# Kernel optimization log

Measured on AMD Instinct MI355X. Metric: run time of the kernel, lower is better.

Reference implementation:

```python
import jax, jax.numpy as jnp
import numpy as np

B, S, H = 2, 2048, 1024
NH, HD = 16, 64  # num heads, head dim
EPS = 1e-12


def setup_inputs() -> dict:
    key = jax.random.key(0)
    ks = jax.random.split(key, 10)
    sc = 1.0 / np.sqrt(H)
    return {
        "hidden_states": jax.random.normal(ks[0], (B, S, H), jnp.float32),
        "Wq": jax.random.normal(ks[1], (H, H), jnp.float32) * sc,
        "bq": jnp.zeros((H,), jnp.float32),
        "Wk": jax.random.normal(ks[2], (H, H), jnp.float32) * sc,
        "bk": jnp.zeros((H,), jnp.float32),
        "Wv": jax.random.normal(ks[3], (H, H), jnp.float32) * sc,
        "bv": jnp.zeros((H,), jnp.float32),
        "Wo": jax.random.normal(ks[4], (H, H), jnp.float32) * sc,
        "bo": jnp.zeros((H,), jnp.float32),
        "ln_g": jnp.ones((H,), jnp.float32),
        "ln_b": jnp.zeros((H,), jnp.float32),
    }


def reference(hidden_states, Wq, bq, Wk, bk, Wv, bv, Wo, bo, ln_g, ln_b):
    x = hidden_states  # [B,S,H]
    def split_heads(t):
        return t.reshape(B, S, NH, HD).transpose(0, 2, 1, 3)  # [B,NH,S,HD]
    q = split_heads(x @ Wq.T + bq)
    k = split_heads(x @ Wk.T + bk)
    v = split_heads(x @ Wv.T + bv)
    scores = jnp.einsum("bhqd,bhkd->bhqk", q, k) / np.sqrt(HD)
    causal = jnp.tril(jnp.ones((S, S), bool))  # [S,S]
    scores = jnp.where(causal[None, None], scores, -jnp.inf)
    probs = jax.nn.softmax(scores, axis=-1)
    ctx = jnp.einsum("bhqk,bhkd->bhqd", probs, v)
    ctx = ctx.transpose(0, 2, 1, 3).reshape(B, S, H)
    attn_out = ctx @ Wo.T + bo
    y = attn_out + x
    mu = jnp.mean(y, axis=-1, keepdims=True)
    var = jnp.mean((y - mu) ** 2, axis=-1, keepdims=True)
    return (y - mu) / jnp.sqrt(var + EPS) * ln_g + ln_b
```

## Files before the change

### kernel.cpp

```cpp
#include <hip/hip_runtime.h>

#define B_  2
#define S_  2048
#define H_  1024
#define NH_ 16
#define HD_ 64
#define M_  (B_*S_)

typedef __attribute__((ext_vector_type(8))) __bf16 bf16x8;
typedef __attribute__((ext_vector_type(4))) float  f32x4;
typedef __attribute__((ext_vector_type(8))) unsigned short us8;
typedef __attribute__((ext_vector_type(4))) float  fl4;

__device__ __forceinline__ unsigned short f2bf(float f) {
    unsigned int u = __float_as_uint(f);
    u += 0x7fffu + ((u >> 16) & 1u);
    return (unsigned short)(u >> 16);
}

__global__ __launch_bounds__(256) void cast_kernel(
    const float* __restrict__ x,
    const float* __restrict__ wq, const float* __restrict__ wk,
    const float* __restrict__ wv, const float* __restrict__ wo,
    unsigned short* __restrict__ xb, unsigned short* __restrict__ wb) {
    size_t t  = (size_t)blockIdx.x * 256 + threadIdx.x;
    size_t e0 = t * 4;
    const size_t XN = (size_t)M_ * H_;
    const float* src;
    unsigned short* dst;
    if (e0 < XN) { src = x + e0; dst = xb + e0; }
    else {
        size_t j = e0 - XN;
        int w = (int)(j >> 20);
        size_t off = j & ((1u << 20) - 1);
        const float* wp = (w == 0) ? wq : (w == 1) ? wk : (w == 2) ? wv : wo;
        src = wp + off; dst = wb + j;
    }
    fl4 v = *(const fl4*)src;
    ushort4 o;
    o.x = f2bf(v.x); o.y = f2bf(v.y); o.z = f2bf(v.z); o.w = f2bf(v.w);
    *(ushort4*)dst = o;
}

__global__ __launch_bounds__(512) void gemm_qkv(
    const unsigned short* __restrict__ xb, const unsigned short* __restrict__ wb,
    const float* __restrict__ bq, const float* __restrict__ bk,
    const float* __restrict__ bv,
    unsigned short* __restrict__ qb, unsigned short* __restrict__ kbuf,
    unsigned short* __restrict__ vT) {
    __shared__ __align__(16) unsigned short As[128 * 72];
    __shared__ __align__(16) unsigned short Bs[128 * 72];
    const int z = blockIdx.z;
    const unsigned short* W = wb + ((size_t)z << 20);
    const int m0 = blockIdx.x * 128, n0 = blockIdx.y * 128;
    const int t = threadIdx.x, lane = t & 63, w = t >> 6;
    const int wm = w >> 2, wn = w & 3;
    const int quad = lane >> 4, l16 = lane & 15;
    const int sr = t >> 2, sc = (t & 3) * 16;
    const unsigned short* ga = xb + (size_t)(m0 + sr) * H_ + sc;
    const unsigned short* gb = W  + (size_t)(n0 + sr) * H_ + sc;

    us8 a0 = *(const us8*)(ga),     a1 = *(const us8*)(ga + 8);
    us8 b0 = *(const us8*)(gb),     b1 = *(const us8*)(gb + 8);

    f32x4 acc[4][2] = {};
    for (int k0 = 0; k0 < H_; k0 += 64) {
        if (k0) __syncthreads();
        *(us8*)&As[sr * 72 + sc]     = a0;  *(us8*)&As[sr * 72 + sc + 8] = a1;
        *(us8*)&Bs[sr * 72 + sc]     = b0;  *(us8*)&Bs[sr * 72 + sc + 8] = b1;
        __syncthreads();
        if (k0 + 64 < H_) {
            ga += 64; gb += 64;
            a0 = *(const us8*)(ga);  a1 = *(const us8*)(ga + 8);
            b0 = *(const us8*)(gb);  b1 = *(const us8*)(gb + 8);
        }
#pragma unroll
        for (int kk = 0; kk < 64; kk += 32) {
            bf16x8 af[4], bfr[2];
#pragma unroll
            for (int i = 0; i < 4; i++)
                af[i]  = *(const bf16x8*)&As[(wm * 64 + i * 16 + l16) * 72 + kk + quad * 8];
#pragma unroll
            for (int jn = 0; jn < 2; jn++)
                bfr[jn] = *(const bf16x8*)&Bs[(wn * 32 + jn * 16 + l16) * 72 + kk + quad * 8];
#pragma unroll
            for (int mi = 0; mi < 4; mi++)
#pragma unroll
                for (int ni = 0; ni < 2; ni++)
                    acc[mi][ni] = __builtin_amdgcn_mfma_f32_16x16x32_bf16(
                        af[mi], bfr[ni], acc[mi][ni], 0, 0, 0);
        }
    }
    const float* bias = (z == 0) ? bq : (z == 1) ? bk : bv;
    if (z == 2) {
#pragma unroll
        for (int mi = 0; mi < 4; mi++) {
#pragma unroll
            for (int ni = 0; ni < 2; ni++) {
                int col  = n0 + wn * 32 + ni * 16 + l16;
                float bval = bias[col];
                int row0 = m0 + wm * 64 + mi * 16 + quad * 4;
                int bb = row0 >> 11, s0 = row0 & 2047;
                ushort4 pk;
                pk.x = f2bf(acc[mi][ni][0] + bval);
                pk.y = f2bf(acc[mi][ni][1] + bval);
                pk.z = f2bf(acc[mi][ni][2] + bval);
                pk.w = f2bf(acc[mi][ni][3] + bval);
                *(ushort4*)&vT[((size_t)bb * NH_ * HD_ + col) * S_ + s0] = pk;
            }
        }
    } else {
        unsigned short* out = (z == 0) ? qb : kbuf;
        const float qs = (z == 0) ? 0.18033688f : 1.0f;
#pragma unroll
        for (int mi = 0; mi < 4; mi++) {
#pragma unroll
            for (int ni = 0; ni < 2; ni++) {
                int col = n0 + wn * 32 + ni * 16 + l16;
                float bval = bias[col];
#pragma unroll
                for (int r = 0; r < 4; r++) {
                    int row = m0 + wm * 64 + mi * 16 + quad * 4 + r;
                    out[(size_t)row * H_ + col] = f2bf((acc[mi][ni][r] + bval) * qs);
                }
            }
        }
    }
}

__global__ __launch_bounds__(512) void gemm_out(
    const unsigned short* __restrict__ ctxb, const unsigned short* __restrict__ wob,
    const float* __restrict__ bo, const float* __restrict__ x,
    float* __restrict__ y) {
    __shared__ __align__(16) unsigned short As[128 * 72];
    __shared__ __align__(16) unsigned short Bs[128 * 72];
    const int m0 = blockIdx.x * 128, n0 = blockIdx.y * 128;
    const int t = threadIdx.x, lane = t & 63, w = t >> 6;
    const int wm = w >> 2, wn = w & 3;
    const int quad = lane >> 4, l16 = lane & 15;
    const int sr = t >> 2, sc = (t & 3) * 16;
    const unsigned short* ga = ctxb + (size_t)(m0 + sr) * H_ + sc;
    const unsigned short* gb = wob  + (size_t)(n0 + sr) * H_ + sc;

    us8 a0 = *(const us8*)(ga),     a1 = *(const us8*)(ga + 8);
    us8 b0 = *(const us8*)(gb),     b1 = *(const us8*)(gb + 8);

    f32x4 acc[4][2] = {};
    for (int k0 = 0; k0 < H_; k0 += 64) {
        if (k0) __syncthreads();
        *(us8*)&As[sr * 72 + sc]     = a0;  *(us8*)&As[sr * 72 + sc + 8] = a1;
        *(us8*)&Bs[sr * 72 + sc]     = b0;  *(us8*)&Bs[sr * 72 + sc + 8] = b1;
        __syncthreads();
        if (k0 + 64 < H_) {
            ga += 64; gb += 64;
            a0 = *(const us8*)(ga);  a1 = *(const us8*)(ga + 8);
            b0 = *(const us8*)(gb);  b1 = *(const us8*)(gb + 8);
        }
#pragma unroll
        for (int kk = 0; kk < 64; kk += 32) {
            bf16x8 af[4], bfr[2];
#pragma unroll
            for (int i = 0; i < 4; i++)
                af[i]  = *(const bf16x8*)&As[(wm * 64 + i * 16 + l16) * 72 + kk + quad * 8];
#pragma unroll
            for (int jn = 0; jn < 2; jn++)
                bfr[jn] = *(const bf16x8*)&Bs[(wn * 32 + jn * 16 + l16) * 72 + kk + quad * 8];
#pragma unroll
            for (int mi = 0; mi < 4; mi++)
#pragma unroll
                for (int ni = 0; ni < 2; ni++)
                    acc[mi][ni] = __builtin_amdgcn_mfma_f32_16x16x32_bf16(
                        af[mi], bfr[ni], acc[mi][ni], 0, 0, 0);
        }
    }
#pragma unroll
    for (int mi = 0; mi < 4; mi++) {
#pragma unroll
        for (int ni = 0; ni < 2; ni++) {
            int col = n0 + wn * 32 + ni * 16 + l16;
            float bval = bo[col];
#pragma unroll
            for (int r = 0; r < 4; r++) {
                size_t idx = (size_t)(m0 + wm * 64 + mi * 16 + quad * 4 + r) * H_ + col;
                y[idx] = acc[mi][ni][r] + bval + x[idx];
            }
        }
    }
}

__global__ __launch_bounds__(512, 4) void attn_kernel(
    const unsigned short* __restrict__ qb, const unsigned short* __restrict__ kb,
    const unsigned short* __restrict__ vT, unsigned short* __restrict__ ctxb) {
    __shared__ __align__(16) unsigned short Ks[2][64 * 72];
    __shared__ __align__(16) unsigned short Vt[2][64 * 72];
    __shared__ __align__(16) unsigned short Ps[128 * 76];
    const int flat = blockIdx.x;
    const int xcd = flat & 7, slot = flat >> 3;
    const int bh  = xcd * 4 + (slot >> 3);
    const int j   = slot & 7;
    const int b = bh >> 4, h = bh & 15;
    const int t = threadIdx.x, lane = t & 63, wid = t >> 6;
    const int grp = wid >> 2, wid4 = wid & 3;
    const int quad = lane >> 4, l16 = lane & 15;
    const int sr8 = t >> 3, sc8 = (t & 7) * 8;
    const size_t headoff = (size_t)h * HD_;
    const unsigned short* vtb = vT + ((size_t)(b * NH_ + h) * HD_) * S_;

    const int p   = j * 2 + grp;
    const int qt1 = p, qt2 = 31 - p;
    const int q01 = qt1 * 64, q02 = qt2 * 64;

    const size_t qr1 = (size_t)(b * S_ + q01 + wid4 * 16 + l16);
    const size_t qr2 = (size_t)(b * S_ + q02 + wid4 * 16 + l16);
    bf16x8 q1a = *(const bf16x8*)(qb + qr1 * H_ + headoff + quad * 8);
    bf16x8 q1b = *(const bf16x8*)(qb + qr1 * H_ + headoff + 32 + quad * 8);
    bf16x8 q2a = *(const bf16x8*)(qb + qr2 * H_ + headoff + quad * 8);
    bf16x8 q2b = *(const bf16x8*)(qb + qr2 * H_ + headoff + 32 + quad * 8);

    float m1 = -1e30f, l1 = 0.f, m2 = -1e30f, l2 = 0.f;
    f32x4 o1[4] = {}, o2[4] = {};

    const unsigned short* kptr = kb  + (size_t)(b * S_ + sr8) * H_ + headoff + sc8;
    const unsigned short* vptr = vtb + (size_t)sr8 * S_ + sc8;
    us8 nk = *(const us8*)kptr;
    us8 nv = *(const us8*)vptr;
    *(us8*)&Ks[0][sr8 * 72 + sc8] = nk;
    *(us8*)&Vt[0][sr8 * 72 + sc8] = nv;
    __syncthreads();

    for (int s = 0; s < 32; s++) {
        const int buf = s & 1;
        const bool pf = (s < 31);
        if (pf) {
            kptr += (size_t)64 * H_;
            vptr += 64;
            nk = *(const us8*)kptr;
            nv = *(const us8*)vptr;
        }
#pragma unroll
        for (int tile = 0; tile < 2; tile++) {
            const int  qt  = tile ? qt2 : qt1;
            if (s > qt) continue;
            const bf16x8 qa = tile ? q2a : q1a;
            const bf16x8 qb_ = tile ? q2b : q1b;
            f32x4 sacc[4] = {};
#pragma unroll
            for (int kk = 0; kk < 64; kk += 32) {
                bf16x8 bqf = (kk == 0) ? qa : qb_;
#pragma unroll
                for (int nt = 0; nt < 4; nt++) {
                    bf16x8 ak = *(const bf16x8*)&Ks[buf][(nt * 16 + l16) * 72 + kk + quad * 8];
                    sacc[nt] = __builtin_amdgcn_mfma_f32_16x16x32_bf16(ak, bqf, sacc[nt], 0, 0, 0);
                }
            }
            if (s == qt) {
#pragma unroll
                for (int nt = 0; nt < 4; nt++) {
#pragma unroll
                    for (int r = 0; r < 4; r++) {
                        int key = nt * 16 + quad * 4 + r;
                        if (key > wid4 * 16 + l16) sacc[nt][r] = -1e30f;
                    }
                }
            }
            float mx = sacc[0][0];
#pragma unroll
            for (int nt = 0; nt < 4; nt++)
#pragma unroll
                for (int r = 0; r < 4; r++) mx = fmaxf(mx, sacc[nt][r]);
            mx = fmaxf(mx, __shfl_xor(mx, 16));
            mx = fmaxf(mx, __shfl_xor(mx, 32));
            float m_old = tile ? m2 : m1;
            float m_new = fmaxf(m_old, mx);
            float alpha = __builtin_amdgcn_exp2f(m_old - m_new);
            float ss = 0.f;
#pragma unroll
            for (int nt = 0; nt < 4; nt++) {
                ushort4 pk;
                float p0 = __builtin_amdgcn_exp2f(sacc[nt][0] - m_new);
                float p1 = __builtin_amdgcn_exp2f(sacc[nt][1] - m_new);
                float p2 = __builtin_amdgcn_exp2f(sacc[nt][2] - m_new);
                float p3 = __builtin_amdgcn_exp2f(sacc[nt][3] - m_new);
                ss += (p0 + p1) + (p2 + p3);
                pk.x = (unsigned short)(__float_as_uint(p0) >> 16);
                pk.y = (unsigned short)(__float_as_uint(p1) >> 16);
                pk.z = (unsigned short)(__float_as_uint(p2) >> 16);
                pk.w = (unsigned short)(__float_as_uint(p3) >> 16);
                *(ushort4*)&Ps[(wid * 16 + l16) * 76 + nt * 16 + quad * 4] = pk;
            }
            ss += __shfl_xor(ss, 16);
            ss += __shfl_xor(ss, 32);
            if (tile) { l2 = l2 * alpha + ss; m2 = m_new; }
            else      { l1 = l1 * alpha + ss; m1 = m_new; }
            f32x4* oo = tile ? o2 : o1;
#pragma unroll
            for (int dt = 0; dt < 4; dt++)
#pragma unroll
                for (int r = 0; r < 4; r++) oo[dt][r] *= alpha;
            __threadfence_block();
#pragma unroll
            for (int kk = 0; kk < 64; kk += 32) {
                bf16x8 pfr = *(const bf16x8*)&Ps[(wid * 16 + l16) * 76 + kk + quad * 8];
#pragma unroll
                for (int dt = 0; dt < 4; dt++) {
                    bf16x8 vf = *(const bf16x8*)&Vt[buf][(dt * 16 + l16) * 72 + kk + quad * 8];
                    oo[dt] = __builtin_amdgcn_mfma_f32_16x16x32_bf16(vf, pfr, oo[dt], 0, 0, 0);
                }
            }
        }
        if (pf) {
            *(us8*)&Ks[buf ^ 1][sr8 * 72 + sc8] = nk;
            *(us8*)&Vt[buf ^ 1][sr8 * 72 + sc8] = nv;
            __syncthreads();
        }
    }
#pragma unroll
    for (int tile = 0; tile < 2; tile++) {
        const int q0 = tile ? q02 : q01;
        const float inv = 1.0f / (tile ? l2 : l1);
        const f32x4* oo = tile ? o2 : o1;
        size_t row = (size_t)(b * S_ + q0 + wid4 * 16 + l16);
#pragma unroll
        for (int dt = 0; dt < 4; dt++) {
            ushort4 pk;
            pk.x = f2bf(oo[dt][0] * inv);
            pk.y = f2bf(oo[dt][1] * inv);
            pk.z = f2bf(oo[dt][2] * inv);
            pk.w = f2bf(oo[dt][3] * inv);
            *(ushort4*)&ctxb[row * H_ + headoff + dt * 16 + quad * 4] = pk;
        }
    }
}

__global__ __launch_bounds__(256) void ln_kernel(
    const float* __restrict__ y, const float* __restrict__ g,
    const float* __restrict__ bta, float* __restrict__ out) {
    __shared__ float red[8];
    const int row = blockIdx.x, t = threadIdx.x;
    fl4 v = *(const fl4*)(y + (size_t)row * H_ + t * 4);
    float s  = v.x + v.y + v.z + v.w;
    float sq = v.x * v.x + v.y * v.y + v.z * v.z + v.w * v.w;
    for (int m = 1; m < 64; m <<= 1) { s += __shfl_xor(s, m); sq += __shfl_xor(sq, m); }
    const int wid = t >> 6, lane = t & 63;
    if (lane == 0) { red[wid * 2] = s; red[wid * 2 + 1] = sq; }
    __syncthreads();
    s  = red[0] + red[2] + red[4] + red[6];
    sq = red[1] + red[3] + red[5] + red[7];
    float mu   = s * (1.0f / H_);
    float var  = sq * (1.0f / H_) - mu * mu;
    float rstd = rsqrtf(fmaxf(var, 0.f) + 1e-12f);
    fl4 gg = *(const fl4*)(g + t * 4);
    fl4 bb = *(const fl4*)(bta + t * 4);
    fl4 o;
    o.x = (v.x - mu) * rstd * gg.x + bb.x;
    o.y = (v.y - mu) * rstd * gg.y + bb.y;
    o.z = (v.z - mu) * rstd * gg.z + bb.z;
    o.w = (v.w - mu) * rstd * gg.w + bb.w;
    *(fl4*)(out + (size_t)row * H_ + t * 4) = o;
}

extern "C" void kernel_launch(void* const* d_in, const int* in_sizes, int n_in,
                              void* d_out, int out_size, void* d_ws, size_t ws_size,
                              hipStream_t stream) {
    const float* x  = (const float*)d_in[0];
    const float* Wq = (const float*)d_in[1];
    const float* bq = (const float*)d_in[2];
    const float* Wk = (const float*)d_in[3];
    const float* bk = (const float*)d_in[4];
    const float* Wv = (const float*)d_in[5];
    const float* bv = (const float*)d_in[6];
    const float* Wo = (const float*)d_in[7];
    const float* bo = (const float*)d_in[8];
    const float* lg = (const float*)d_in[9];
    const float* lb = (const float*)d_in[10];
    float* out = (float*)d_out;

    const size_t MEG = 1024u * 1024u;
    unsigned short* ws16 = (unsigned short*)d_ws;
    unsigned short* xb   = ws16;
    unsigned short* wb   = ws16 + 4 * MEG;
    unsigned short* qb   = ws16 + 8 * MEG;
    unsigned short* kb   = ws16 + 12 * MEG;
    unsigned short* vT   = ws16 + 16 * MEG;
    unsigned short* ctxb = ws16 + 20 * MEG;
    float* y = (float*)(ws16 + 24 * MEG);

    cast_kernel<<<8192, 256, 0, stream>>>(x, Wq, Wk, Wv, Wo, xb, wb);
    gemm_qkv<<<dim3(32, 8, 3), 512, 0, stream>>>(xb, wb, bq, bk, bv, qb, kb, vT);
    attn_kernel<<<dim3(256), 512, 0, stream>>>(qb, kb, vT, ctxb);
    gemm_out<<<dim3(32, 8), 512, 0, stream>>>(ctxb, wb + 3 * MEG, bo, x, y);
    ln_kernel<<<4096, 256, 0, stream>>>(y, lg, lb, out);
}
```

Measured before the change: 194.4 us.

## Split attention query-tile pairs across wave groups and double the grid

Each block previously had both wave groups walk a pair of query tiles (p, 31-p) in turn over all 32 key steps. Now each group owns a single query tile: group 0 takes tile p and group 1 takes tile 31-p. The block runs only 32-p key steps and the grid doubles to 512 blocks. This halves per-wave accumulator state and sequential work and puts more waves in flight for latency hiding. The cost is that the short-tile group idles at the shared barriers while the long-tile group finishes.

```diff
diff --git a/kernel.cpp b/kernel.cpp
--- a/kernel.cpp
+++ b/kernel.cpp
@@ -196,8 +196,8 @@
     __shared__ __align__(16) unsigned short Ps[128 * 76];
     const int flat = blockIdx.x;
     const int xcd = flat & 7, slot = flat >> 3;
-    const int bh  = xcd * 4 + (slot >> 3);
-    const int j   = slot & 7;
+    const int bh  = xcd * 4 + (slot >> 4);
+    const int p   = slot & 15;
     const int b = bh >> 4, h = bh & 15;
     const int t = threadIdx.x, lane = t & 63, wid = t >> 6;
     const int grp = wid >> 2, wid4 = wid & 3;
@@ -206,19 +206,16 @@
     const size_t headoff = (size_t)h * HD_;
     const unsigned short* vtb = vT + ((size_t)(b * NH_ + h) * HD_) * S_;
 
-    const int p   = j * 2 + grp;
-    const int qt1 = p, qt2 = 31 - p;
-    const int q01 = qt1 * 64, q02 = qt2 * 64;
-
-    const size_t qr1 = (size_t)(b * S_ + q01 + wid4 * 16 + l16);
-    const size_t qr2 = (size_t)(b * S_ + q02 + wid4 * 16 + l16);
-    bf16x8 q1a = *(const bf16x8*)(qb + qr1 * H_ + headoff + quad * 8);
-    bf16x8 q1b = *(const bf16x8*)(qb + qr1 * H_ + headoff + 32 + quad * 8);
-    bf16x8 q2a = *(const bf16x8*)(qb + qr2 * H_ + headoff + quad * 8);
-    bf16x8 q2b = *(const bf16x8*)(qb + qr2 * H_ + headoff + 32 + quad * 8);
-
-    float m1 = -1e30f, l1 = 0.f, m2 = -1e30f, l2 = 0.f;
-    f32x4 o1[4] = {}, o2[4] = {};
+    const int qt = grp ? (31 - p) : p;
+    const int q0 = qt * 64;
+    const int nsteps = 32 - p;
+
+    const size_t qr = (size_t)(b * S_ + q0 + wid4 * 16 + l16);
+    bf16x8 qva = *(const bf16x8*)(qb + qr * H_ + headoff + quad * 8);
+    bf16x8 qvb = *(const bf16x8*)(qb + qr * H_ + headoff + 32 + quad * 8);
+
+    float m1 = -1e30f, l1 = 0.f;
+    f32x4 o1[4] = {};
 
     const unsigned short* kptr = kb  + (size_t)(b * S_ + sr8) * H_ + headoff + sc8;
     const unsigned short* vptr = vtb + (size_t)sr8 * S_ + sc8;
@@ -228,25 +225,20 @@
     *(us8*)&Vt[0][sr8 * 72 + sc8] = nv;
     __syncthreads();
 
-    for (int s = 0; s < 32; s++) {
+    for (int s = 0; s < nsteps; s++) {
         const int buf = s & 1;
-        const bool pf = (s < 31);
+        const bool pf = (s + 1 < nsteps);
         if (pf) {
             kptr += (size_t)64 * H_;
             vptr += 64;
             nk = *(const us8*)kptr;
             nv = *(const us8*)vptr;
         }
-#pragma unroll
-        for (int tile = 0; tile < 2; tile++) {
-            const int  qt  = tile ? qt2 : qt1;
-            if (s > qt) continue;
-            const bf16x8 qa = tile ? q2a : q1a;
-            const bf16x8 qb_ = tile ? q2b : q1b;
+        if (s <= qt) {
             f32x4 sacc[4] = {};
 #pragma unroll
             for (int kk = 0; kk < 64; kk += 32) {
-                bf16x8 bqf = (kk == 0) ? qa : qb_;
+                bf16x8 bqf = (kk == 0) ? qva : qvb;
 #pragma unroll
                 for (int nt = 0; nt < 4; nt++) {
                     bf16x8 ak = *(const bf16x8*)&Ks[buf][(nt * 16 + l16) * 72 + kk + quad * 8];
@@ -270,9 +262,8 @@
                 for (int r = 0; r < 4; r++) mx = fmaxf(mx, sacc[nt][r]);
             mx = fmaxf(mx, __shfl_xor(mx, 16));
             mx = fmaxf(mx, __shfl_xor(mx, 32));
-            float m_old = tile ? m2 : m1;
-            float m_new = fmaxf(m_old, mx);
-            float alpha = __builtin_amdgcn_exp2f(m_old - m_new);
+            float m_new = fmaxf(m1, mx);
+            float alpha = __builtin_amdgcn_exp2f(m1 - m_new);
             float ss = 0.f;
 #pragma unroll
             for (int nt = 0; nt < 4; nt++) {
@@ -290,13 +281,12 @@
             }
             ss += __shfl_xor(ss, 16);
             ss += __shfl_xor(ss, 32);
-            if (tile) { l2 = l2 * alpha + ss; m2 = m_new; }
-            else      { l1 = l1 * alpha + ss; m1 = m_new; }
-            f32x4* oo = tile ? o2 : o1;
+            l1 = l1 * alpha + ss;
+            m1 = m_new;
 #pragma unroll
             for (int dt = 0; dt < 4; dt++)
 #pragma unroll
-                for (int r = 0; r < 4; r++) oo[dt][r] *= alpha;
+                for (int r = 0; r < 4; r++) o1[dt][r] *= alpha;
             __threadfence_block();
 #pragma unroll
             for (int kk = 0; kk < 64; kk += 32) {
@@ -304,7 +294,7 @@
 #pragma unroll
                 for (int dt = 0; dt < 4; dt++) {
                     bf16x8 vf = *(const bf16x8*)&Vt[buf][(dt * 16 + l16) * 72 + kk + quad * 8];
-                    oo[dt] = __builtin_amdgcn_mfma_f32_16x16x32_bf16(vf, pfr, oo[dt], 0, 0, 0);
+                    o1[dt] = __builtin_amdgcn_mfma_f32_16x16x32_bf16(vf, pfr, o1[dt], 0, 0, 0);
                 }
             }
         }
@@ -314,19 +304,16 @@
             __syncthreads();
         }
     }
-#pragma unroll
-    for (int tile = 0; tile < 2; tile++) {
-        const int q0 = tile ? q02 : q01;
-        const float inv = 1.0f / (tile ? l2 : l1);
-        const f32x4* oo = tile ? o2 : o1;
+    {
+        const float inv = 1.0f / l1;
         size_t row = (size_t)(b * S_ + q0 + wid4 * 16 + l16);
 #pragma unroll
         for (int dt = 0; dt < 4; dt++) {
             ushort4 pk;
-            pk.x = f2bf(oo[dt][0] * inv);
-            pk.y = f2bf(oo[dt][1] * inv);
-            pk.z = f2bf(oo[dt][2] * inv);
-            pk.w = f2bf(oo[dt][3] * inv);
+            pk.x = f2bf(o1[dt][0] * inv);
+            pk.y = f2bf(o1[dt][1] * inv);
+            pk.z = f2bf(o1[dt][2] * inv);
+            pk.w = f2bf(o1[dt][3] * inv);
             *(ushort4*)&ctxb[row * H_ + headoff + dt * 16 + quad * 4] = pk;
         }
     }
@@ -387,7 +374,7 @@
 
     cast_kernel<<<8192, 256, 0, stream>>>(x, Wq, Wk, Wv, Wo, xb, wb);
     gemm_qkv<<<dim3(32, 8, 3), 512, 0, stream>>>(xb, wb, bq, bk, bv, qb, kb, vT);
-    attn_kernel<<<dim3(256), 512, 0, stream>>>(qb, kb, vT, ctxb);
+    attn_kernel<<<dim3(512), 512, 0, stream>>>(qb, kb, vT, ctxb);
     gemm_out<<<dim3(32, 8), 512, 0, stream>>>(ctxb, wb + 3 * MEG, bo, x, y);
     ln_kernel<<<4096, 256, 0, stream>>>(y, lg, lb, out);
 }
```

Result: slower. 198.4 us (+2.1%).
